# Optimization experiments

Measured on AMD Instinct MI355X. Metric: run time of the kernel, lower is better.

The kernel has to match this reference:

```python
import jax, jax.numpy as jnp
import numpy as np


def setup_inputs() -> dict:
    num_nodes = 524288  # 2**19
    embedding_dim = 128
    batch = 65536
    key = jax.random.key(0)
    k1, k2, k3, k4 = jax.random.split(key, 4)
    return {
        "center": jax.random.randint(k1, (batch,), 0, num_nodes, dtype=jnp.int32),
        "context": jax.random.randint(k2, (batch,), 0, num_nodes, dtype=jnp.int32),
        "embeddings": jax.random.normal(k3, (num_nodes, embedding_dim), dtype=jnp.float32),
        "probs_tensor": jax.random.uniform(k4, (2 * num_nodes, embedding_dim), dtype=jnp.float32),
    }


def reference(center, context, embeddings, probs_tensor):
    num_nodes = embeddings.shape[0]
    # leaf ids in the implicit binary tree: [num_nodes, 2*num_nodes-1]
    context_node = context + num_nodes  # [B]
    # num_nodes is a power of two, so every path has length L = log2(num_nodes)
    # (length_binary == floor(log2(context_node)) == L for all leaves).
    L = int(np.log2(num_nodes))
    # torch loop runs i in range(1, L): tree nodes context_node >> i, i=1..L-1
    levels = jnp.arange(1, L, dtype=jnp.int32)  # [L-1]
    nodes = context_node[:, None] >> levels[None, :]  # [B, L-1] internal path ids
    signs = jnp.where(nodes % 2 == 0, 1.0, -1.0).astype(embeddings.dtype)  # [B, L-1]
    embed_center = embeddings[center]  # [B, D]
    gathered = probs_tensor[nodes]  # [B, L-1, D]
    dot = jnp.einsum("bld,bd->bl", gathered, embed_center)  # [B, L-1]
    # log(sigmoid(s*x)) accumulated over the path, stable form
    logp = jnp.sum(jax.nn.log_sigmoid(signs * dot), axis=1, keepdims=True)  # [B, 1]
    return -logp
```

## Files before the change

kernel.cpp:

```cpp
#include <hip/hip_runtime.h>


#define HS_NUM_NODES (1 << 19)
#define HS_LVLS 18

template <int N, int M>
__device__ inline void fold_step(float* w, int sub) {
    const bool hi = (sub & M) != 0;
    constexpr int NN = (N + 1) / 2;
#pragma unroll
    for (int k = 0; k < NN; ++k) {
        const float a = w[2 * k];
        const float b = (2 * k + 1 < N) ? w[2 * k + 1] : 0.f;
        const float keep = hi ? b : a;
        const float send = hi ? a : b;
        w[k] = keep + __shfl_xor(send, M, 64);
    }
}

__global__ __launch_bounds__(256) void hs_fwd_kernel(
    const int* __restrict__ center,
    const int* __restrict__ context,
    const float* __restrict__ emb,
    const float* __restrict__ probs,
    float* __restrict__ out,
    int B)
{
    const int tid  = blockIdx.x * blockDim.x + threadIdx.x;
    const int elem = tid >> 5;
    if (elem >= B) return;
    const int sub = threadIdx.x & 31;

    const int c   = center[elem];
    const int ctx = context[elem] + HS_NUM_NODES;

    const float4 ec =
        *reinterpret_cast<const float4*>(emb + (size_t)c * 128 + sub * 4);

    float4 p[HS_LVLS];
#pragma unroll
    for (int i = 0; i < HS_LVLS; ++i) {
        const int node = ctx >> (i + 1);
        p[i] = *reinterpret_cast<const float4*>(
            probs + (size_t)node * 128 + sub * 4);
    }

    float w[HS_LVLS];
#pragma unroll
    for (int i = 0; i < HS_LVLS; ++i)
        w[i] = p[i].x * ec.x + p[i].y * ec.y + p[i].z * ec.z + p[i].w * ec.w;

    fold_step<18, 1>(w, sub);
    fold_step<9,  2>(w, sub);
    fold_step<5,  4>(w, sub);
    fold_step<3,  8>(w, sub);
    fold_step<2, 16>(w, sub);

    const int sh   = (sub < HS_LVLS) ? (sub + 1) : 1;
    const int node = ctx >> sh;
    const float S  = w[0];
    const float x  = (node & 1) ? -S : S;
    float ls = fminf(x, 0.f) - __logf(1.f + __expf(-fabsf(x)));
    ls = (sub < HS_LVLS) ? ls : 0.f;

    float acc = ls;
#pragma unroll
    for (int m = 16; m; m >>= 1) acc += __shfl_xor(acc, m, 64);

    if (sub == 0) out[elem] = -acc;
}

extern "C" void kernel_launch(void* const* d_in, const int* in_sizes, int n_in,
                              void* d_out, int out_size, void* d_ws, size_t ws_size,
                              hipStream_t stream) {
    const int*   center  = (const int*)d_in[0];
    const int*   context = (const int*)d_in[1];
    const float* emb     = (const float*)d_in[2];
    const float* probs   = (const float*)d_in[3];
    float*       out     = (float*)d_out;

    const int B = in_sizes[0];
    const int threads = 256;
    const int blocks  = (B * 32 + threads - 1) / threads;
    hs_fwd_kernel<<<blocks, threads, 0, stream>>>(center, context, emb, probs,
                                                  out, B);
}
```

Before: 48.23 us.

## Map each batch element to a full 64-lane wavefront with float2 loads

Each element is now handled by a full 64-lane wavefront instead of a 32-lane half. Each lane loads float2 slices rather than float4, so the per-thread register array for the 18 path rows halves. An extra shuffle fold stage and a wider final reduction cover the 64 lanes, and launch bounds now request 8 blocks per CU. The aim is higher occupancy and more outstanding random gathers to hide memory latency, at the cost of twice the threads and more shuffle and instruction overhead per element.

Result: slower. 51.13 us (+6.0%).

```diff
diff --git a/kernel.cpp b/kernel.cpp
--- a/kernel.cpp
+++ b/kernel.cpp
@@ -5,8 +5,8 @@
 #define HS_LVLS 18
 
 template <int N, int M>
-__device__ inline void fold_step(float* w, int sub) {
-    const bool hi = (sub & M) != 0;
+__device__ inline void fold_step(float* w, int lane) {
+    const bool hi = (lane & M) != 0;
     constexpr int NN = (N + 1) / 2;
 #pragma unroll
     for (int k = 0; k < NN; ++k) {
@@ -18,7 +18,7 @@
     }
 }
 
-__global__ __launch_bounds__(256) void hs_fwd_kernel(
+__global__ __launch_bounds__(256, 8) void hs_fwd_kernel(
     const int* __restrict__ center,
     const int* __restrict__ context,
     const float* __restrict__ emb,
@@ -26,48 +26,48 @@
     float* __restrict__ out,
     int B)
 {
-    const int tid  = blockIdx.x * blockDim.x + threadIdx.x;
-    const int elem = tid >> 5;
+    const int elem = blockIdx.x * (blockDim.x >> 6) + (threadIdx.x >> 6);
     if (elem >= B) return;
-    const int sub = threadIdx.x & 31;
+    const int lane = threadIdx.x & 63;
 
     const int c   = center[elem];
     const int ctx = context[elem] + HS_NUM_NODES;
 
-    const float4 ec =
-        *reinterpret_cast<const float4*>(emb + (size_t)c * 128 + sub * 4);
+    const float2 ec =
+        *reinterpret_cast<const float2*>(emb + (size_t)c * 128 + lane * 2);
 
-    float4 p[HS_LVLS];
+    float2 p[HS_LVLS];
 #pragma unroll
     for (int i = 0; i < HS_LVLS; ++i) {
         const int node = ctx >> (i + 1);
-        p[i] = *reinterpret_cast<const float4*>(
-            probs + (size_t)node * 128 + sub * 4);
+        p[i] = *reinterpret_cast<const float2*>(
+            probs + (size_t)node * 128 + lane * 2);
     }
 
     float w[HS_LVLS];
 #pragma unroll
     for (int i = 0; i < HS_LVLS; ++i)
-        w[i] = p[i].x * ec.x + p[i].y * ec.y + p[i].z * ec.z + p[i].w * ec.w;
+        w[i] = p[i].x * ec.x + p[i].y * ec.y;
 
-    fold_step<18, 1>(w, sub);
-    fold_step<9,  2>(w, sub);
-    fold_step<5,  4>(w, sub);
-    fold_step<3,  8>(w, sub);
-    fold_step<2, 16>(w, sub);
+    fold_step<18, 1>(w, lane);
+    fold_step<9,  2>(w, lane);
+    fold_step<5,  4>(w, lane);
+    fold_step<3,  8>(w, lane);
+    fold_step<2, 16>(w, lane);
+    fold_step<1, 32>(w, lane);
 
-    const int sh   = (sub < HS_LVLS) ? (sub + 1) : 1;
+    const int sh   = (lane < HS_LVLS) ? (lane + 1) : 1;
     const int node = ctx >> sh;
     const float S  = w[0];
     const float x  = (node & 1) ? -S : S;
     float ls = fminf(x, 0.f) - __logf(1.f + __expf(-fabsf(x)));
-    ls = (sub < HS_LVLS) ? ls : 0.f;
+    ls = (lane < HS_LVLS) ? ls : 0.f;
 
     float acc = ls;
 #pragma unroll
-    for (int m = 16; m; m >>= 1) acc += __shfl_xor(acc, m, 64);
+    for (int m = 32; m; m >>= 1) acc += __shfl_xor(acc, m, 64);
 
-    if (sub == 0) out[elem] = -acc;
+    if (lane == 0) out[elem] = -acc;
 }
 
 extern "C" void kernel_launch(void* const* d_in, const int* in_sizes, int n_in,
@@ -81,7 +81,7 @@
 
     const int B = in_sizes[0];
     const int threads = 256;
-    const int blocks  = (B * 32 + threads - 1) / threads;
+    const int blocks  = (B * 64 + threads - 1) / threads;
     hs_fwd_kernel<<<blocks, threads, 0, stream>>>(center, context, emb, probs,
                                                   out, B);
 }
```

## Bucket-sort batch elements by context before the gather to improve path locality

Applied to the files above, without the earlier changes.

Adds a histogram, scan and scatter pass that builds a permutation grouping batch elements by high bits of their context id. The main kernel processes elements in that order so nearby elements share tree-path rows in cache. It also remaps block ids so consecutive blocks spread across XCDs, each XCD taking a contiguous range of buckets. The cost is three extra small kernels plus a memset and an extra indirection per element, and the output write becomes scattered.

Result: slower. 68.06 us (+41.1%).

```diff
diff --git a/kernel.cpp b/kernel.cpp
--- a/kernel.cpp
+++ b/kernel.cpp
@@ -3,6 +3,8 @@
 
 #define HS_NUM_NODES (1 << 19)
 #define HS_LVLS 18
+#define HS_NBKT 1024
+#define HS_BSH  9
 
 template <int N, int M>
 __device__ inline void fold_step(float* w, int sub) {
@@ -18,18 +20,54 @@
     }
 }
 
+__global__ void hs_hist(const int* __restrict__ ctx, int B,
+                        int* __restrict__ hist) {
+    const int i = blockIdx.x * blockDim.x + threadIdx.x;
+    if (i < B) atomicAdd(&hist[ctx[i] >> HS_BSH], 1);
+}
+
+__global__ __launch_bounds__(HS_NBKT) void hs_scan(int* __restrict__ hist) {
+    __shared__ int a[HS_NBKT], b[HS_NBKT];
+    const int t = threadIdx.x;
+    const int orig = hist[t];
+    a[t] = orig;
+    __syncthreads();
+    int* src = a; int* dst = b;
+#pragma unroll
+    for (int off = 1; off < HS_NBKT; off <<= 1) {
+        dst[t] = (t >= off) ? (src[t] + src[t - off]) : src[t];
+        __syncthreads();
+        int* tmp = src; src = dst; dst = tmp;
+    }
+    hist[t] = src[t] - orig;
+}
+
+__global__ void hs_scatter(const int* __restrict__ ctx, int B,
+                           int* __restrict__ off, int* __restrict__ perm) {
+    const int i = blockIdx.x * blockDim.x + threadIdx.x;
+    if (i < B) {
+        const int p = atomicAdd(&off[ctx[i] >> HS_BSH], 1);
+        perm[p] = i;
+    }
+}
+
 __global__ __launch_bounds__(256) void hs_fwd_kernel(
     const int* __restrict__ center,
     const int* __restrict__ context,
     const float* __restrict__ emb,
     const float* __restrict__ probs,
+    const int* __restrict__ perm,
     float* __restrict__ out,
     int B)
 {
-    const int tid  = blockIdx.x * blockDim.x + threadIdx.x;
-    const int elem = tid >> 5;
-    if (elem >= B) return;
-    const int sub = threadIdx.x & 31;
+    int bid = blockIdx.x;
+    const int nb = gridDim.x;
+    if ((nb & 7) == 0) bid = (bid & 7) * (nb >> 3) + (bid >> 3);
+
+    const int slot = bid * (blockDim.x >> 5) + (threadIdx.x >> 5);
+    if (slot >= B) return;
+    const int elem = perm ? perm[slot] : slot;
+    const int sub  = threadIdx.x & 31;
 
     const int c   = center[elem];
     const int ctx = context[elem] + HS_NUM_NODES;
@@ -82,6 +120,18 @@
     const int B = in_sizes[0];
     const int threads = 256;
     const int blocks  = (B * 32 + threads - 1) / threads;
+
+    const size_t ws_need = (size_t)(HS_NBKT + B) * sizeof(int);
+    int* perm = nullptr;
+    if (ws_size >= ws_need) {
+        int* hist = (int*)d_ws;
+        perm      = hist + HS_NBKT;
+        hipMemsetAsync(hist, 0, HS_NBKT * sizeof(int), stream);
+        hs_hist   <<<(B + 255) / 256, 256, 0, stream>>>(context, B, hist);
+        hs_scan   <<<1, HS_NBKT, 0, stream>>>(hist);
+        hs_scatter<<<(B + 255) / 256, 256, 0, stream>>>(context, B, hist, perm);
+    }
+
     hs_fwd_kernel<<<blocks, threads, 0, stream>>>(center, context, emb, probs,
-                                                  out, B);
+                                                  perm, out, B);
 }
```

## Cache top tree levels of probs in LDS with persistent grid-stride blocks

Applied to the files above, without the earlier changes.

Copies the 126 internal nodes at the top six tree levels (nodes 2..127) into shared memory once per block. Each of the 256 persistent 1024-thread blocks then grid-strides over batch elements, reading 12 levels from global memory and 6 from LDS. The aim is to cut redundant global and L2 traffic for these heavily shared upper nodes. In exchange it uses about 63KB of LDS per block, which limits occupancy, and adds a one-time fill plus a block-wide barrier.

New measurement: 50.00 us. +3.7%, slower.

```diff
diff --git a/kernel.cpp b/kernel.cpp
--- a/kernel.cpp
+++ b/kernel.cpp
@@ -3,6 +3,9 @@
 
 #define HS_NUM_NODES (1 << 19)
 #define HS_LVLS 18
+#define HS_GLB  12
+#define HS_LDSL 6
+#define HS_LDS_FLOATS (126 * 128)
 
 template <int N, int M>
 __device__ inline void fold_step(float* w, int sub) {
@@ -18,7 +21,7 @@
     }
 }
 
-__global__ __launch_bounds__(256) void hs_fwd_kernel(
+__global__ __launch_bounds__(1024) void hs_fwd_kernel(
     const int* __restrict__ center,
     const int* __restrict__ context,
     const float* __restrict__ emb,
@@ -26,48 +29,70 @@
     float* __restrict__ out,
     int B)
 {
-    const int tid  = blockIdx.x * blockDim.x + threadIdx.x;
-    const int elem = tid >> 5;
-    if (elem >= B) return;
-    const int sub = threadIdx.x & 31;
+    __shared__ float lds[HS_LDS_FLOATS];
 
-    const int c   = center[elem];
-    const int ctx = context[elem] + HS_NUM_NODES;
+    {
+        const float4* src = reinterpret_cast<const float4*>(probs) + 64;
+        float4*       dst = reinterpret_cast<float4*>(lds);
+        for (int k = threadIdx.x; k < HS_LDS_FLOATS / 4; k += 1024)
+            dst[k] = src[k];
+    }
+    __syncthreads();
 
-    const float4 ec =
-        *reinterpret_cast<const float4*>(emb + (size_t)c * 128 + sub * 4);
+    const int group = threadIdx.x >> 5;
+    const int sub   = threadIdx.x & 31;
+    const int ngroups = gridDim.x * 32;
 
-    float4 p[HS_LVLS];
+    for (int slot = blockIdx.x * 32 + group; slot < B; slot += ngroups) {
+        const int c   = center[slot];
+        const int ctx = context[slot] + HS_NUM_NODES;
+
+        const float4 ec =
+            *reinterpret_cast<const float4*>(emb + (size_t)c * 128 + sub * 4);
+
+        float4 p[HS_GLB];
 #pragma unroll
-    for (int i = 0; i < HS_LVLS; ++i) {
-        const int node = ctx >> (i + 1);
-        p[i] = *reinterpret_cast<const float4*>(
-            probs + (size_t)node * 128 + sub * 4);
+        for (int i = 0; i < HS_GLB; ++i) {
+            const int node = ctx >> (i + 1);
+            p[i] = *reinterpret_cast<const float4*>(
+                probs + (size_t)node * 128 + sub * 4);
+        }
+        float4 q[HS_LDSL];
+#pragma unroll
+        for (int i = 0; i < HS_LDSL; ++i) {
+            const int node = ctx >> (i + 13);
+            q[i] = *reinterpret_cast<const float4*>(
+                lds + (node - 2) * 128 + sub * 4);
+        }
+
+        float w[HS_LVLS];
+#pragma unroll
+        for (int i = 0; i < HS_GLB; ++i)
+            w[i] = p[i].x * ec.x + p[i].y * ec.y + p[i].z * ec.z + p[i].w * ec.w;
+#pragma unroll
+        for (int i = 0; i < HS_LDSL; ++i)
+            w[HS_GLB + i] = q[i].x * ec.x + q[i].y * ec.y
+                          + q[i].z * ec.z + q[i].w * ec.w;
+
+        fold_step<18, 1>(w, sub);
+        fold_step<9,  2>(w, sub);
+        fold_step<5,  4>(w, sub);
+        fold_step<3,  8>(w, sub);
+        fold_step<2, 16>(w, sub);
+
+        const int sh   = (sub < HS_LVLS) ? (sub + 1) : 1;
+        const int node = ctx >> sh;
+        const float S  = w[0];
+        const float x  = (node & 1) ? -S : S;
+        float ls = fminf(x, 0.f) - __logf(1.f + __expf(-fabsf(x)));
+        ls = (sub < HS_LVLS) ? ls : 0.f;
+
+        float acc = ls;
+#pragma unroll
+        for (int m = 16; m; m >>= 1) acc += __shfl_xor(acc, m, 64);
+
+        if (sub == 0) out[slot] = -acc;
     }
-
-    float w[HS_LVLS];
-#pragma unroll
-    for (int i = 0; i < HS_LVLS; ++i)
-        w[i] = p[i].x * ec.x + p[i].y * ec.y + p[i].z * ec.z + p[i].w * ec.w;
-
-    fold_step<18, 1>(w, sub);
-    fold_step<9,  2>(w, sub);
-    fold_step<5,  4>(w, sub);
-    fold_step<3,  8>(w, sub);
-    fold_step<2, 16>(w, sub);
-
-    const int sh   = (sub < HS_LVLS) ? (sub + 1) : 1;
-    const int node = ctx >> sh;
-    const float S  = w[0];
-    const float x  = (node & 1) ? -S : S;
-    float ls = fminf(x, 0.f) - __logf(1.f + __expf(-fabsf(x)));
-    ls = (sub < HS_LVLS) ? ls : 0.f;
-
-    float acc = ls;
-#pragma unroll
-    for (int m = 16; m; m >>= 1) acc += __shfl_xor(acc, m, 64);
-
-    if (sub == 0) out[elem] = -acc;
 }
 
 extern "C" void kernel_launch(void* const* d_in, const int* in_sizes, int n_in,
@@ -80,8 +105,6 @@
     float*       out     = (float*)d_out;
 
     const int B = in_sizes[0];
-    const int threads = 256;
-    const int blocks  = (B * 32 + threads - 1) / threads;
-    hs_fwd_kernel<<<blocks, threads, 0, stream>>>(center, context, emb, probs,
-                                                  out, B);
+    hs_fwd_kernel<<<256, 1024, 0, stream>>>(center, context, emb, probs,
+                                            out, B);
 }
```
